# Optimization experiments

Measured on AMD Instinct MI355X. Metric: run time of the kernel, lower is better.

## Reference

```python
import jax, jax.numpy as jnp
import numpy as np

N = 8192          # number of latent vectors z
M = 16384         # number of KDE sample points (multiple of N_EMB)
N_EMB = 16        # n_embeddings on the circle
Z_DIM = 2         # fixed by get_embeddings (cos/sin stack)
INIT_LOG_SIGMA = 0.0


def setup_inputs() -> dict:
    key = jax.random.key(0)
    k1, k2 = jax.random.split(key)
    z = jax.random.normal(k1, (N, Z_DIM), dtype=jnp.float32)
    eps = jax.random.normal(k2, (M // N_EMB, Z_DIM), dtype=jnp.float32)
    # get_embeddings: points on a circle of radius 4
    angles = jnp.linspace(0.0, 2.0 * np.pi, N_EMB)
    embeddings = (jnp.stack([jnp.cos(angles), jnp.sin(angles)], axis=1) * 4.0).astype(jnp.float32)
    log_sigma = jnp.full((1,), INIT_LOG_SIGMA, dtype=jnp.float32)
    temperature = jnp.full((1,), 0.5, dtype=jnp.float32)
    return {"z": z, "embeddings": embeddings, "log_sigma": log_sigma,
            "eps": eps, "temperature": temperature}


def reference(z, embeddings, log_sigma, eps, temperature):
    T = temperature[0]
    ls = log_sigma[0]
    sigma = jnp.exp(ls)
    z_dim = z.shape[1]
    n = z.shape[0]
    # mean: (n_emb, D); samples e: (n_emb * M//n_emb, D) == (M, D)
    mean = (1.0 - T) * embeddings
    e = (mean[:, None, :] + eps[None, :, :] * T).reshape(-1, z_dim)
    # squared euclidean distance (N, M) via gemm expansion (same math as ||z-e||^2)
    d = (jnp.sum(z * z, axis=1)[:, None]
         + jnp.sum(e * e, axis=1)[None, :]
         - 2.0 * (z @ e.T))
    alpha = -1.0 / (2.0 * sigma ** 2)
    lse = jax.nn.logsumexp(alpha * d, axis=0)  # reduce over N -> (M,)
    # np.log(np.e) == 1.0
    loss = (-jnp.mean(lse)
            + 0.5 * z_dim * (2.0 * ls - 1.0)
            + jnp.log(jnp.float32(n)))
    return loss
```

## Files before the change

### kernel.cpp

```cpp
#include <hip/hip_runtime.h>
#include <math.h>

#define N_TOT 8192
#define M_TOT 16384
#define EPS_N 1024
#define N_EMB 16

#define LOG2E 1.4426950408889634f
#define LN2   0.6931471805599453f
#define EXP2(x) __builtin_amdgcn_exp2f(x)
#define LOG2F_(x) __builtin_amdgcn_logf(x)

#define BLOCK 256
#define IC    128
#define NICH  (N_TOT / IC)
#define LCH   128
#define NLCH  (EPS_N / LCH)

__global__ __launch_bounds__(BLOCK) void gemm_partial_kernel(
    const float* __restrict__ z, const float* __restrict__ emb,
    const float* __restrict__ log_sigma, const float* __restrict__ eps,
    const float* __restrict__ temperature, float* __restrict__ part)
{
    __shared__ float4 rows[IC * 5];
    __shared__ float red[4][N_EMB * LCH];

    const int t  = threadIdx.x;
    const int l0 = blockIdx.x * LCH;
    const int ib = blockIdx.y;

    const float ls = log_sigma[0];
    const float T  = temperature[0];
    const float alpha = -0.5f * EXP2(LOG2E * (-2.0f * ls));
    const float La  = LOG2E * alpha;
    const float omT = 1.0f - T;

    {
        const int il = t & (IC - 1);
        const int kh = t >> 7;
        const int i  = ib * IC + il;
        const float z0 = z[2 * i], z1 = z[2 * i + 1];
        const float c  = La * (z0 * z0 + z1 * z1);
        const float b0 = -2.0f * La * z0, b1 = -2.0f * La * z1;
        float4 pa, pb;
#pragma unroll
        for (int kk = 0; kk < 4; ++kk) {
            int k = kh * 8 + kk;
            float m0 = omT * emb[2 * k], m1 = omT * emb[2 * k + 1];
            ((float*)&pa)[kk] = EXP2(c + b0 * m0 + b1 * m1);
        }
#pragma unroll
        for (int kk = 0; kk < 4; ++kk) {
            int k = kh * 8 + 4 + kk;
            float m0 = omT * emb[2 * k], m1 = omT * emb[2 * k + 1];
            ((float*)&pb)[kk] = EXP2(c + b0 * m0 + b1 * m1);
        }
        rows[il * 5 + kh * 2]     = pa;
        rows[il * 5 + kh * 2 + 1] = pb;
        if (kh == 0)
            rows[il * 5 + 4] = make_float4(T * b0, T * b1, 0.0f, 0.0f);
    }

    const int lane = t & 63;
    const int w    = t >> 6;
    const float2* eps2 = (const float2*)eps;
    const float2 ua = eps2[l0 + lane];
    const float2 ub = eps2[l0 + 64 + lane];

    __syncthreads();

    float sa[N_EMB] = {0.0f};
    float sb[N_EMB] = {0.0f};
#pragma unroll 2
    for (int n = 0; n < IC / 4; ++n) {
        const int ir = w * (IC / 4) + n;
        float4 p0 = rows[ir * 5 + 0];
        float4 p1 = rows[ir * 5 + 1];
        float4 p2 = rows[ir * 5 + 2];
        float4 p3 = rows[ir * 5 + 3];
        float4 tb = rows[ir * 5 + 4];
        float qa = EXP2(fmaf(tb.y, ua.y, tb.x * ua.x));
        float qb = EXP2(fmaf(tb.y, ub.y, tb.x * ub.x));
        float pk[16];
        *(float4*)&pk[0]  = p0; *(float4*)&pk[4]  = p1;
        *(float4*)&pk[8]  = p2; *(float4*)&pk[12] = p3;
#pragma unroll
        for (int k = 0; k < N_EMB; ++k) {
            sa[k] = fmaf(pk[k], qa, sa[k]);
            sb[k] = fmaf(pk[k], qb, sb[k]);
        }
    }

#pragma unroll
    for (int k = 0; k < N_EMB; ++k) {
        red[w][k * LCH + lane]      = sa[k];
        red[w][k * LCH + 64 + lane] = sb[k];
    }
    __syncthreads();
#pragma unroll
    for (int r = 0; r < (N_EMB * LCH) / BLOCK; ++r) {
        const int e  = t + r * BLOCK;
        const float S = red[0][e] + red[1][e] + red[2][e] + red[3][e];
        const int k  = e >> 7;
        const int lc = e & (LCH - 1);
        part[ib * M_TOT + k * EPS_N + l0 + lc] = S;
    }
}

__global__ __launch_bounds__(BLOCK) void reduce_kernel(
    const float* __restrict__ emb, const float* __restrict__ log_sigma,
    const float* __restrict__ eps, const float* __restrict__ temperature,
    const float* __restrict__ part, float* __restrict__ bsum)
{
    const int j = blockIdx.x * BLOCK + threadIdx.x;
    const float ls = log_sigma[0];
    const float T  = temperature[0];
    const float alpha = -0.5f * EXP2(LOG2E * (-2.0f * ls));

    float S = 0.0f;
#pragma unroll 8
    for (int ib = 0; ib < NICH; ++ib)
        S += part[ib * M_TOT + j];

    const int k = j >> 10, l = j & (EPS_N - 1);
    const float omT = 1.0f - T;
    const float e0 = omT * emb[2 * k]     + T * eps[2 * l];
    const float e1 = omT * emb[2 * k + 1] + T * eps[2 * l + 1];
    const float g  = LOG2E * alpha * (e0 * e0 + e1 * e1);

    float v = g + LOG2F_(S);

#pragma unroll
    for (int off = 32; off; off >>= 1) v += __shfl_down(v, off, 64);
    __shared__ float wsum[BLOCK / 64];
    const int lane = threadIdx.x & 63, w = threadIdx.x >> 6;
    if (lane == 0) wsum[w] = v;
    __syncthreads();
    if (threadIdx.x == 0)
        bsum[blockIdx.x] = wsum[0] + wsum[1] + wsum[2] + wsum[3];
}

__global__ void final_kernel(const float* __restrict__ log_sigma,
                             const float* __restrict__ bsum,
                             float* __restrict__ out)
{
    float v = bsum[threadIdx.x];
#pragma unroll
    for (int off = 32; off; off >>= 1) v += __shfl_down(v, off, 64);
    if (threadIdx.x == 0) {
        const float ls = log_sigma[0];
        const float sum_lse = v * LN2;
        out[0] = -sum_lse / (float)M_TOT + (2.0f * ls - 1.0f) + 9.010913347279288f;
    }
}

extern "C" void kernel_launch(void* const* d_in, const int* in_sizes, int n_in,
                              void* d_out, int out_size, void* d_ws, size_t ws_size,
                              hipStream_t stream)
{
    const float* z    = (const float*)d_in[0];
    const float* emb  = (const float*)d_in[1];
    const float* lsig = (const float*)d_in[2];
    const float* eps  = (const float*)d_in[3];
    const float* temp = (const float*)d_in[4];

    float* part = (float*)d_ws;
    float* bsum = part + (size_t)NICH * M_TOT;

    dim3 grid1(NLCH, NICH);
    gemm_partial_kernel<<<grid1, BLOCK, 0, stream>>>(z, emb, lsig, eps, temp, part);
    reduce_kernel<<<M_TOT / BLOCK, BLOCK, 0, stream>>>(emb, lsig, eps, temp, part, bsum);
    final_kernel<<<1, 64, 0, stream>>>(lsig, bsum, (float*)d_out);
}
```

Baseline: 73.95 us.

## Widen eps tile per block, use LDS atomics, fuse final reduction into reduce kernel

The first kernel now uses 512 threads and 256 eps columns per block, so each wave processes 16 z rows against 4 eps columns. This doubles reuse of the exp'd row factors, and the four-way LDS reduction buffer is replaced by a zero-initialised tile accumulated with shared-memory atomicAdd. The final single-block kernel is removed: the last block of the reduce kernel, found with a global atomic counter and threadfence, sums the 64 block sums. This saves a launch and cuts per-element exp work, but it adds LDS atomic contention and a higher register count from the 64 accumulators per thread.

```diff
diff --git a/kernel.cpp b/kernel.cpp
--- a/kernel.cpp
+++ b/kernel.cpp
@@ -8,26 +8,30 @@
 
 #define LOG2E 1.4426950408889634f
 #define LN2   0.6931471805599453f
-#define EXP2(x) __builtin_amdgcn_exp2f(x)
+#define EXP2(x)   __builtin_amdgcn_exp2f(x)
 #define LOG2F_(x) __builtin_amdgcn_logf(x)
 
-#define BLOCK 256
+#define BLK1  512
 #define IC    128
 #define NICH  (N_TOT / IC)
-#define LCH   128
+#define LCH   256
 #define NLCH  (EPS_N / LCH)
+#define NQ    (LCH / 64)
 
-__global__ __launch_bounds__(BLOCK) void gemm_partial_kernel(
+__global__ __launch_bounds__(BLK1) void gemm_partial_kernel(
     const float* __restrict__ z, const float* __restrict__ emb,
     const float* __restrict__ log_sigma, const float* __restrict__ eps,
-    const float* __restrict__ temperature, float* __restrict__ part)
+    const float* __restrict__ temperature, float* __restrict__ part,
+    unsigned int* __restrict__ counter)
 {
-    __shared__ float4 rows[IC * 5];
-    __shared__ float red[4][N_EMB * LCH];
+    __shared__ __align__(16) float4 rows[IC * 5];
+    __shared__ __align__(16) float  tile[N_EMB * LCH];
 
     const int t  = threadIdx.x;
     const int l0 = blockIdx.x * LCH;
     const int ib = blockIdx.y;
+
+    if (blockIdx.x == 0 && ib == 0 && t == 0) *counter = 0u;
 
     const float ls = log_sigma[0];
     const float T  = temperature[0];
@@ -37,82 +41,89 @@
 
     {
         const int il = t & (IC - 1);
-        const int kh = t >> 7;
+        const int kq = t >> 7;
         const int i  = ib * IC + il;
         const float z0 = z[2 * i], z1 = z[2 * i + 1];
         const float c  = La * (z0 * z0 + z1 * z1);
         const float b0 = -2.0f * La * z0, b1 = -2.0f * La * z1;
-        float4 pa, pb;
+        float4 p;
 #pragma unroll
         for (int kk = 0; kk < 4; ++kk) {
-            int k = kh * 8 + kk;
-            float m0 = omT * emb[2 * k], m1 = omT * emb[2 * k + 1];
-            ((float*)&pa)[kk] = EXP2(c + b0 * m0 + b1 * m1);
+            const int k = kq * 4 + kk;
+            const float m0 = omT * emb[2 * k], m1 = omT * emb[2 * k + 1];
+            ((float*)&p)[kk] = EXP2(c + b0 * m0 + b1 * m1);
         }
-#pragma unroll
-        for (int kk = 0; kk < 4; ++kk) {
-            int k = kh * 8 + 4 + kk;
-            float m0 = omT * emb[2 * k], m1 = omT * emb[2 * k + 1];
-            ((float*)&pb)[kk] = EXP2(c + b0 * m0 + b1 * m1);
-        }
-        rows[il * 5 + kh * 2]     = pa;
-        rows[il * 5 + kh * 2 + 1] = pb;
-        if (kh == 0)
-            rows[il * 5 + 4] = make_float4(T * b0, T * b1, 0.0f, 0.0f);
+        rows[il * 5 + kq] = p;
+        if (kq == 0) rows[il * 5 + 4] = make_float4(T * b0, T * b1, 0.0f, 0.0f);
+
+        const float4 z4 = make_float4(0.0f, 0.0f, 0.0f, 0.0f);
+        ((float4*)tile)[t * 2]     = z4;
+        ((float4*)tile)[t * 2 + 1] = z4;
     }
 
     const int lane = t & 63;
     const int w    = t >> 6;
     const float2* eps2 = (const float2*)eps;
-    const float2 ua = eps2[l0 + lane];
-    const float2 ub = eps2[l0 + 64 + lane];
+    float2 u[NQ];
+#pragma unroll
+    for (int q = 0; q < NQ; ++q) u[q] = eps2[l0 + lane + 64 * q];
 
     __syncthreads();
 
-    float sa[N_EMB] = {0.0f};
-    float sb[N_EMB] = {0.0f};
-#pragma unroll 2
-    for (int n = 0; n < IC / 4; ++n) {
-        const int ir = w * (IC / 4) + n;
-        float4 p0 = rows[ir * 5 + 0];
-        float4 p1 = rows[ir * 5 + 1];
-        float4 p2 = rows[ir * 5 + 2];
-        float4 p3 = rows[ir * 5 + 3];
-        float4 tb = rows[ir * 5 + 4];
-        float qa = EXP2(fmaf(tb.y, ua.y, tb.x * ua.x));
-        float qb = EXP2(fmaf(tb.y, ub.y, tb.x * ub.x));
-        float pk[16];
+    float acc[N_EMB][NQ];
+#pragma unroll
+    for (int k = 0; k < N_EMB; ++k)
+#pragma unroll
+        for (int q = 0; q < NQ; ++q) acc[k][q] = 0.0f;
+
+    const int ibase = w * (IC / 8);
+    for (int n = 0; n < IC / 8; ++n) {
+        const int ir = ibase + n;
+        const float4 p0 = rows[ir * 5 + 0];
+        const float4 p1 = rows[ir * 5 + 1];
+        const float4 p2 = rows[ir * 5 + 2];
+        const float4 p3 = rows[ir * 5 + 3];
+        const float4 tb = rows[ir * 5 + 4];
+        float qv[NQ];
+#pragma unroll
+        for (int q = 0; q < NQ; ++q)
+            qv[q] = EXP2(fmaf(tb.y, u[q].y, tb.x * u[q].x));
+        float pk[N_EMB];
         *(float4*)&pk[0]  = p0; *(float4*)&pk[4]  = p1;
         *(float4*)&pk[8]  = p2; *(float4*)&pk[12] = p3;
 #pragma unroll
-        for (int k = 0; k < N_EMB; ++k) {
-            sa[k] = fmaf(pk[k], qa, sa[k]);
-            sb[k] = fmaf(pk[k], qb, sb[k]);
-        }
+        for (int k = 0; k < N_EMB; ++k)
+#pragma unroll
+            for (int q = 0; q < NQ; ++q)
+                acc[k][q] = fmaf(pk[k], qv[q], acc[k][q]);
     }
 
 #pragma unroll
-    for (int k = 0; k < N_EMB; ++k) {
-        red[w][k * LCH + lane]      = sa[k];
-        red[w][k * LCH + 64 + lane] = sb[k];
-    }
+    for (int k = 0; k < N_EMB; ++k)
+#pragma unroll
+        for (int q = 0; q < NQ; ++q)
+            atomicAdd(&tile[k * LCH + lane + 64 * q], acc[k][q]);
     __syncthreads();
-#pragma unroll
-    for (int r = 0; r < (N_EMB * LCH) / BLOCK; ++r) {
-        const int e  = t + r * BLOCK;
-        const float S = red[0][e] + red[1][e] + red[2][e] + red[3][e];
-        const int k  = e >> 7;
-        const int lc = e & (LCH - 1);
-        part[ib * M_TOT + k * EPS_N + l0 + lc] = S;
+
+    {
+        const int base = t * 8;
+        const int k  = base >> 8;
+        const int lo = base & (LCH - 1);
+        float* dst = part + (size_t)ib * M_TOT + k * EPS_N + l0 + lo;
+        ((float4*)dst)[0] = ((float4*)tile)[t * 2];
+        ((float4*)dst)[1] = ((float4*)tile)[t * 2 + 1];
     }
 }
 
-__global__ __launch_bounds__(BLOCK) void reduce_kernel(
+#define BLK2 256
+__global__ __launch_bounds__(BLK2) void reduce_final_kernel(
     const float* __restrict__ emb, const float* __restrict__ log_sigma,
     const float* __restrict__ eps, const float* __restrict__ temperature,
-    const float* __restrict__ part, float* __restrict__ bsum)
+    const float* __restrict__ part, float* __restrict__ sc,
+    unsigned int* __restrict__ counter, float* __restrict__ out)
 {
-    const int j = blockIdx.x * BLOCK + threadIdx.x;
+    const int t = threadIdx.x;
+    const int j = blockIdx.x * BLK2 + t;
     const float ls = log_sigma[0];
     const float T  = temperature[0];
     const float alpha = -0.5f * EXP2(LOG2E * (-2.0f * ls));
@@ -120,7 +131,7 @@
     float S = 0.0f;
 #pragma unroll 8
     for (int ib = 0; ib < NICH; ++ib)
-        S += part[ib * M_TOT + j];
+        S += part[(size_t)ib * M_TOT + j];
 
     const int k = j >> 10, l = j & (EPS_N - 1);
     const float omT = 1.0f - T;
@@ -132,25 +143,29 @@
 
 #pragma unroll
     for (int off = 32; off; off >>= 1) v += __shfl_down(v, off, 64);
-    __shared__ float wsum[BLOCK / 64];
-    const int lane = threadIdx.x & 63, w = threadIdx.x >> 6;
+    __shared__ float wsum[BLK2 / 64];
+    const int lane = t & 63, w = t >> 6;
     if (lane == 0) wsum[w] = v;
     __syncthreads();
-    if (threadIdx.x == 0)
-        bsum[blockIdx.x] = wsum[0] + wsum[1] + wsum[2] + wsum[3];
-}
 
-__global__ void final_kernel(const float* __restrict__ log_sigma,
-                             const float* __restrict__ bsum,
-                             float* __restrict__ out)
-{
-    float v = bsum[threadIdx.x];
+    __shared__ int is_last;
+    if (t == 0) {
+        sc[blockIdx.x] = wsum[0] + wsum[1] + wsum[2] + wsum[3];
+        __threadfence();
+        unsigned int old = atomicAdd(counter, 1u);
+        is_last = (old == (unsigned)(M_TOT / BLK2 - 1));
+    }
+    __syncthreads();
+
+    if (is_last && t < 64) {
+        __threadfence();
+        float x = sc[t];
 #pragma unroll
-    for (int off = 32; off; off >>= 1) v += __shfl_down(v, off, 64);
-    if (threadIdx.x == 0) {
-        const float ls = log_sigma[0];
-        const float sum_lse = v * LN2;
-        out[0] = -sum_lse / (float)M_TOT + (2.0f * ls - 1.0f) + 9.010913347279288f;
+        for (int off = 32; off; off >>= 1) x += __shfl_down(x, off, 64);
+        if (t == 0) {
+            const float sum_lse = x * LN2;
+            out[0] = -sum_lse / (float)M_TOT + (2.0f * ls - 1.0f) + 9.010913347279288f;
+        }
     }
 }
 
@@ -164,11 +179,12 @@
     const float* eps  = (const float*)d_in[3];
     const float* temp = (const float*)d_in[4];
 
-    float* part = (float*)d_ws;
-    float* bsum = part + (size_t)NICH * M_TOT;
+    float*        part    = (float*)d_ws;
+    float*        sc      = part + (size_t)NICH * M_TOT;
+    unsigned int* counter = (unsigned int*)(sc + 64);
 
     dim3 grid1(NLCH, NICH);
-    gemm_partial_kernel<<<grid1, BLOCK, 0, stream>>>(z, emb, lsig, eps, temp, part);
-    reduce_kernel<<<M_TOT / BLOCK, BLOCK, 0, stream>>>(emb, lsig, eps, temp, part, bsum);
-    final_kernel<<<1, 64, 0, stream>>>(lsig, bsum, (float*)d_out);
+    gemm_partial_kernel<<<grid1, BLK1, 0, stream>>>(z, emb, lsig, eps, temp, part, counter);
+    reduce_final_kernel<<<M_TOT / BLK2, BLK2, 0, stream>>>(emb, lsig, eps, temp, part, sc,
+                                                           counter, (float*)d_out);
 }
```

Result: slower. 115.0 us (+55.5%).
